# Kernel optimization log

Hardware: AMD Instinct MI355X
Metric: run time of the kernel (lower is better)

The kernel has to match this reference:

```python
import math
import jax, jax.numpy as jnp
import numpy as np

TOP_K = 2
N_EXP = 8
TRAIN_CAPACITY = 1.25
MIN_CAPACITY = 4


def _capacity(num_tokens):
    cap = math.floor(TOP_K * TRAIN_CAPACITY * num_tokens / N_EXP)
    cap += cap % 2
    return max(cap, MIN_CAPACITY)


def _router(x, w_g):
    B, T, D = x.shape
    N = B * T
    C = _capacity(N)  # static: depends only on shapes

    logits = jnp.einsum('btd,ed->bte', x, w_g)            # [B,T,E]
    _, top_idx = jax.lax.top_k(logits, TOP_K)             # [B,T,K]
    probs = jax.nn.softmax(logits, axis=-1).reshape(N, N_EXP)  # [N,E]
    idx = top_idx.reshape(N, TOP_K)                       # [N,K]

    # one-hot expert mask, laid out [K, N, E] as in the torch code
    exp_mask = jax.nn.one_hot(idx, N_EXP, dtype=jnp.int32)      # [N,K,E]
    exp_mask = jnp.transpose(exp_mask, (1, 0, 2))               # [K,N,E]

    # position of each routed token within its expert's queue
    rank = jnp.cumsum(exp_mask.reshape(TOP_K * N, N_EXP), axis=0)
    rank = rank.reshape(TOP_K, N, N_EXP) - 1                    # [K,N,E]

    exp_mask = exp_mask * (rank < C).astype(jnp.int32)          # drop over-capacity
    used_capacity = jnp.sum(exp_mask, axis=(0, 1))              # [E]
    rank_sel = jnp.sum(exp_mask * rank, axis=-1)                # [K,N] int

    idx_kn = jnp.transpose(idx)                                 # [K,N]
    keep = jnp.take_along_axis(exp_mask, idx_kn[:, :, None], axis=2)[..., 0]  # [K,N]
    p_sel = jnp.transpose(jnp.take_along_axis(probs, idx, axis=1))            # [K,N]
    w = keep.astype(probs.dtype) * p_sel                        # [K,N]

    # cb_weight[n, e, c] = sum_k exp_weights[k,n,e] * one_hot(rank_sel)[k,n,c]
    # implemented as a direct scatter-add instead of materializing the
    # O(K*N*E*C) outer product (dropped tokens contribute weight 0).
    tok = jnp.arange(N)
    cb_weight = jnp.zeros((N, N_EXP, C), probs.dtype)
    cb_weight = cb_weight.at[tok[None, :], idx_kn, rank_sel].add(w)
    sec_mask = cb_weight != 0
    return used_capacity, cb_weight, sec_mask


def setup_inputs() -> dict:
    key = jax.random.key(0)
    kx, kw = jax.random.split(key)
    x = jax.random.normal(kx, (2, 2048, 1024), dtype=jnp.float32)
    w_g = jax.random.normal(kw, (8, 1024), dtype=jnp.float32) * 0.02
    return {"x": x, "w_g": w_g}


def reference(x, w_g):
    return _router(x, w_g)
```

## Files before the change

### kernel.cpp

```cpp
#include <hip/hip_runtime.h>

#define N_TOK 4096
#define DIM   1024
#define NE    8
#define CAP   1280
#define EC    (NE * CAP)
#define NEC   ((size_t)N_TOK * EC)

__global__ __launch_bounds__(256) void k_logits(const float* __restrict__ x,
                                                const float* __restrict__ wg,
                                                int* __restrict__ top_idx,
                                                float* __restrict__ top_p) {
    __shared__ float swg[NE * DIM];
    const float4* wg4 = (const float4*)wg;
    float4* swg4 = (float4*)swg;
#pragma unroll
    for (int i = 0; i < 8; ++i) {
        int t = i * 256 + threadIdx.x;
        swg4[t] = wg4[t];
    }
    __syncthreads();

    const int wave = threadIdx.x >> 6;
    const int lane = threadIdx.x & 63;
    const int token = blockIdx.x * 4 + wave;

    const float4* x4 = (const float4*)(x + (size_t)token * DIM);
    float acc[NE];
#pragma unroll
    for (int e = 0; e < NE; ++e) acc[e] = 0.f;

#pragma unroll
    for (int c = 0; c < 4; ++c) {
        float4 xv = x4[c * 64 + lane];
#pragma unroll
        for (int e = 0; e < NE; ++e) {
            float4 wv = swg4[e * 256 + c * 64 + lane];
            acc[e] += xv.x * wv.x + xv.y * wv.y + xv.z * wv.z + xv.w * wv.w;
        }
    }
#pragma unroll
    for (int e = 0; e < NE; ++e) {
        float v = acc[e];
#pragma unroll
        for (int off = 32; off > 0; off >>= 1)
            v += __shfl_xor(v, off, 64);
        acc[e] = v;
    }

    if (lane == 0) {
        float m = acc[0];
#pragma unroll
        for (int e = 1; e < NE; ++e) m = fmaxf(m, acc[e]);
        float pe[NE];
        float s = 0.f;
#pragma unroll
        for (int e = 0; e < NE; ++e) { pe[e] = expf(acc[e] - m); s += pe[e]; }
        float inv = 1.f / s;

        int i1 = 0; float v1 = acc[0];
#pragma unroll
        for (int e = 1; e < NE; ++e) if (acc[e] > v1) { v1 = acc[e]; i1 = e; }
        int i2 = (i1 == 0) ? 1 : 0; float v2 = acc[i2];
#pragma unroll
        for (int e = 0; e < NE; ++e)
            if (e != i1 && acc[e] > v2) { v2 = acc[e]; i2 = e; }

        top_idx[token]         = i1;
        top_idx[N_TOK + token] = i2;
        top_p[token]           = pe[i1] * inv;
        top_p[N_TOK + token]   = pe[i2] * inv;
    }
}

__global__ __launch_bounds__(256) void k_rank(const int* __restrict__ top_idx,
                                              int* __restrict__ dest,
                                              float* __restrict__ used) {
    __shared__ int se[2 * N_TOK];
    __shared__ int wsum[4][NE];
    const int t = threadIdx.x;
    const int lane = t & 63;
    const int wave = t >> 6;

    const int4* ti4 = (const int4*)top_idx;
    int4* se4 = (int4*)se;
#pragma unroll
    for (int i = 0; i < 8; ++i)
        se4[i * 256 + t] = ti4[i * 256 + t];
    __syncthreads();

    int cnt[NE];
#pragma unroll
    for (int e = 0; e < NE; ++e) cnt[e] = 0;
    const int base = t * 32;
#pragma unroll
    for (int jj = 0; jj < 32; ++jj) {
        int v = se[base + jj];
#pragma unroll
        for (int e = 0; e < NE; ++e) cnt[e] += (v == e) ? 1 : 0;
    }

    int incl[NE];
#pragma unroll
    for (int e = 0; e < NE; ++e) {
        int s = cnt[e];
#pragma unroll
        for (int off = 1; off < 64; off <<= 1) {
            int u = __shfl_up(s, off, 64);
            if (lane >= off) s += u;
        }
        incl[e] = s;
        if (lane == 63) wsum[wave][e] = s;
    }
    __syncthreads();

    int excl[NE];
#pragma unroll
    for (int e = 0; e < NE; ++e) {
        int off = 0;
#pragma unroll
        for (int w = 0; w < 4; ++w)
            off += (w < wave) ? wsum[w][e] : 0;
        excl[e] = off + incl[e] - cnt[e];
    }
    if (t < NE) {
        int total = wsum[0][t] + wsum[1][t] + wsum[2][t] + wsum[3][t];
        used[t] = (float)min(total, CAP);
    }

    int run[NE];
#pragma unroll
    for (int e = 0; e < NE; ++e) run[e] = excl[e];
#pragma unroll
    for (int jj = 0; jj < 32; ++jj) {
        int j = base + jj;
        int v = se[j];
        int r = run[0];
#pragma unroll
        for (int e = 1; e < NE; ++e) r = (v == e) ? run[e] : r;
#pragma unroll
        for (int e = 0; e < NE; ++e) run[e] += (v == e) ? 1 : 0;
        dest[j] = (r < CAP) ? (v * CAP + r) : -1;
    }
}

__global__ __launch_bounds__(256) void k_scatter(const int* __restrict__ dest,
                                                 const float* __restrict__ top_p,
                                                 const float* __restrict__ used,
                                                 float* __restrict__ out) {
    const int j = blockIdx.x * 256 + threadIdx.x;
    if (blockIdx.x == 0 && threadIdx.x < NE) out[threadIdx.x] = used[threadIdx.x];

    const int d = dest[j];
    if (d >= 0) {
        const int n = j & (N_TOK - 1);
        const float w = top_p[j];
        out[8 + (size_t)n * EC + d]       = w;
        out[8 + NEC + (size_t)n * EC + d] = (w != 0.f) ? 1.f : 0.f;
    }
}

extern "C" void kernel_launch(void* const* d_in, const int* in_sizes, int n_in,
                              void* d_out, int out_size, void* d_ws, size_t ws_size,
                              hipStream_t stream) {
    const float* x  = (const float*)d_in[0];
    const float* wg = (const float*)d_in[1];
    float* out = (float*)d_out;
    char* ws = (char*)d_ws;

    int*   top_idx = (int*)(ws);
    float* top_p   = (float*)(ws + 32768);
    int*   dest    = (int*)(ws + 65536);
    float* used    = (float*)(ws + 98304);

    hipMemsetAsync(out, 0, (size_t)(8 + 2 * NEC) * sizeof(float), stream);

    k_logits<<<N_TOK / 4, 256, 0, stream>>>(x, wg, top_idx, top_p);
    k_rank<<<1, 256, 0, stream>>>(top_idx, dest, used);
    k_scatter<<<2 * N_TOK / 256, 256, 0, stream>>>(dest, top_p, used, out);
}
```

Before: 356.4 us.

## Fuse output zero-fill into logits kernel and merge rank with scatter

Replaces the hipMemsetAsync of the large output with a zero-fill done by 2048 blocks of the logits kernel, where the first 1024 blocks also compute the router logits. The rank and scatter kernels are merged into one single-block kernel that keeps destinations in shared memory. The goal is to cut launch count and overlap the bandwidth-bound zero fill with the logits compute. In exchange, the fill pattern is hand-sized and the scatter now runs in a single block, which serialises about 8K stores.

```diff
diff --git a/kernel.cpp b/kernel.cpp
--- a/kernel.cpp
+++ b/kernel.cpp
@@ -7,76 +7,99 @@
 #define EC    (NE * CAP)
 #define NEC   ((size_t)N_TOK * EC)
 
-__global__ __launch_bounds__(256) void k_logits(const float* __restrict__ x,
-                                                const float* __restrict__ wg,
-                                                int* __restrict__ top_idx,
-                                                float* __restrict__ top_p) {
+#define NB_FILL   2048
+#define F4_TOTAL  ((2 * NEC + 8) / 4)
+#define F4_BLOCK  (40 * 256)
+#define F4_MAIN   ((size_t)NB_FILL * F4_BLOCK)
+
+typedef float nt_float4 __attribute__((ext_vector_type(4)));
+
+__global__ __launch_bounds__(256) void k_fill_logits(const float* __restrict__ x,
+                                                     const float* __restrict__ wg,
+                                                     int* __restrict__ top_idx,
+                                                     float* __restrict__ top_p,
+                                                     float* __restrict__ out) {
     __shared__ float swg[NE * DIM];
-    const float4* wg4 = (const float4*)wg;
-    float4* swg4 = (float4*)swg;
+    const int bid = blockIdx.x;
+    const int tid = threadIdx.x;
+
+    if (bid < N_TOK / 4) {
+        const float4* wg4 = (const float4*)wg;
+        float4* swg4 = (float4*)swg;
 #pragma unroll
-    for (int i = 0; i < 8; ++i) {
-        int t = i * 256 + threadIdx.x;
-        swg4[t] = wg4[t];
-    }
-    __syncthreads();
+        for (int i = 0; i < 8; ++i) {
+            int t = i * 256 + tid;
+            swg4[t] = wg4[t];
+        }
+        __syncthreads();
 
-    const int wave = threadIdx.x >> 6;
-    const int lane = threadIdx.x & 63;
-    const int token = blockIdx.x * 4 + wave;
+        const int wave = tid >> 6;
+        const int lane = tid & 63;
+        const int token = bid * 4 + wave;
 
-    const float4* x4 = (const float4*)(x + (size_t)token * DIM);
-    float acc[NE];
+        const float4* x4 = (const float4*)(x + (size_t)token * DIM);
+        float acc[NE];
 #pragma unroll
-    for (int e = 0; e < NE; ++e) acc[e] = 0.f;
+        for (int e = 0; e < NE; ++e) acc[e] = 0.f;
 
 #pragma unroll
-    for (int c = 0; c < 4; ++c) {
-        float4 xv = x4[c * 64 + lane];
+        for (int c = 0; c < 4; ++c) {
+            float4 xv = x4[c * 64 + lane];
+#pragma unroll
+            for (int e = 0; e < NE; ++e) {
+                float4 wv = swg4[e * 256 + c * 64 + lane];
+                acc[e] += xv.x * wv.x + xv.y * wv.y + xv.z * wv.z + xv.w * wv.w;
+            }
+        }
 #pragma unroll
         for (int e = 0; e < NE; ++e) {
-            float4 wv = swg4[e * 256 + c * 64 + lane];
-            acc[e] += xv.x * wv.x + xv.y * wv.y + xv.z * wv.z + xv.w * wv.w;
+            float v = acc[e];
+#pragma unroll
+            for (int off = 32; off > 0; off >>= 1)
+                v += __shfl_xor(v, off, 64);
+            acc[e] = v;
+        }
+
+        if (lane == 0) {
+            float m = acc[0];
+#pragma unroll
+            for (int e = 1; e < NE; ++e) m = fmaxf(m, acc[e]);
+            float pe[NE];
+            float s = 0.f;
+#pragma unroll
+            for (int e = 0; e < NE; ++e) { pe[e] = expf(acc[e] - m); s += pe[e]; }
+            float inv = 1.f / s;
+
+            int i1 = 0; float v1 = acc[0];
+#pragma unroll
+            for (int e = 1; e < NE; ++e) if (acc[e] > v1) { v1 = acc[e]; i1 = e; }
+            int i2 = (i1 == 0) ? 1 : 0; float v2 = acc[i2];
+#pragma unroll
+            for (int e = 0; e < NE; ++e)
+                if (e != i1 && acc[e] > v2) { v2 = acc[e]; i2 = e; }
+
+            top_idx[token]         = i1;
+            top_idx[N_TOK + token] = i2;
+            top_p[token]           = pe[i1] * inv;
+            top_p[N_TOK + token]   = pe[i2] * inv;
         }
     }
+
+    nt_float4 z = (nt_float4)0.f;
+    nt_float4* o4 = (nt_float4*)out;
+    const size_t base = (size_t)bid * F4_BLOCK + tid;
 #pragma unroll
-    for (int e = 0; e < NE; ++e) {
-        float v = acc[e];
-#pragma unroll
-        for (int off = 32; off > 0; off >>= 1)
-            v += __shfl_xor(v, off, 64);
-        acc[e] = v;
-    }
-
-    if (lane == 0) {
-        float m = acc[0];
-#pragma unroll
-        for (int e = 1; e < NE; ++e) m = fmaxf(m, acc[e]);
-        float pe[NE];
-        float s = 0.f;
-#pragma unroll
-        for (int e = 0; e < NE; ++e) { pe[e] = expf(acc[e] - m); s += pe[e]; }
-        float inv = 1.f / s;
-
-        int i1 = 0; float v1 = acc[0];
-#pragma unroll
-        for (int e = 1; e < NE; ++e) if (acc[e] > v1) { v1 = acc[e]; i1 = e; }
-        int i2 = (i1 == 0) ? 1 : 0; float v2 = acc[i2];
-#pragma unroll
-        for (int e = 0; e < NE; ++e)
-            if (e != i1 && acc[e] > v2) { v2 = acc[e]; i2 = e; }
-
-        top_idx[token]         = i1;
-        top_idx[N_TOK + token] = i2;
-        top_p[token]           = pe[i1] * inv;
-        top_p[N_TOK + token]   = pe[i2] * inv;
-    }
+    for (int i = 0; i < 40; ++i)
+        o4[base + i * 256] = z;
+    if (bid == 0 && tid < (int)(F4_TOTAL - F4_MAIN))
+        o4[F4_MAIN + tid] = z;
 }
 
-__global__ __launch_bounds__(256) void k_rank(const int* __restrict__ top_idx,
-                                              int* __restrict__ dest,
-                                              float* __restrict__ used) {
+__global__ __launch_bounds__(256) void k_rank_scatter(const int* __restrict__ top_idx,
+                                                      const float* __restrict__ top_p,
+                                                      float* __restrict__ out) {
     __shared__ int se[2 * N_TOK];
+    __shared__ int sdest[2 * N_TOK];
     __shared__ int wsum[4][NE];
     const int t = threadIdx.x;
     const int lane = t & 63;
@@ -125,7 +148,7 @@
     }
     if (t < NE) {
         int total = wsum[0][t] + wsum[1][t] + wsum[2][t] + wsum[3][t];
-        used[t] = (float)min(total, CAP);
+        out[t] = (float)min(total, CAP);
     }
 
     int run[NE];
@@ -140,23 +163,20 @@
         for (int e = 1; e < NE; ++e) r = (v == e) ? run[e] : r;
 #pragma unroll
         for (int e = 0; e < NE; ++e) run[e] += (v == e) ? 1 : 0;
-        dest[j] = (r < CAP) ? (v * CAP + r) : -1;
+        sdest[j] = (r < CAP) ? (v * CAP + r) : -1;
     }
-}
+    __syncthreads();
 
-__global__ __launch_bounds__(256) void k_scatter(const int* __restrict__ dest,
-                                                 const float* __restrict__ top_p,
-                                                 const float* __restrict__ used,
-                                                 float* __restrict__ out) {
-    const int j = blockIdx.x * 256 + threadIdx.x;
-    if (blockIdx.x == 0 && threadIdx.x < NE) out[threadIdx.x] = used[threadIdx.x];
-
-    const int d = dest[j];
-    if (d >= 0) {
-        const int n = j & (N_TOK - 1);
-        const float w = top_p[j];
-        out[8 + (size_t)n * EC + d]       = w;
-        out[8 + NEC + (size_t)n * EC + d] = (w != 0.f) ? 1.f : 0.f;
+#pragma unroll
+    for (int jj = 0; jj < 32; ++jj) {
+        int j = jj * 256 + t;
+        int d = sdest[j];
+        if (d >= 0) {
+            int n = j & (N_TOK - 1);
+            float w = top_p[j];
+            out[8 + (size_t)n * EC + d]       = w;
+            out[8 + NEC + (size_t)n * EC + d] = (w != 0.f) ? 1.f : 0.f;
+        }
     }
 }
 
@@ -170,12 +190,7 @@
 
     int*   top_idx = (int*)(ws);
     float* top_p   = (float*)(ws + 32768);
-    int*   dest    = (int*)(ws + 65536);
-    float* used    = (float*)(ws + 98304);
 
-    hipMemsetAsync(out, 0, (size_t)(8 + 2 * NEC) * sizeof(float), stream);
-
-    k_logits<<<N_TOK / 4, 256, 0, stream>>>(x, wg, top_idx, top_p);
-    k_rank<<<1, 256, 0, stream>>>(top_idx, dest, used);
-    k_scatter<<<2 * N_TOK / 256, 256, 0, stream>>>(dest, top_p, used, out);
+    k_fill_logits<<<NB_FILL, 256, 0, stream>>>(x, wg, top_idx, top_p, out);
+    k_rank_scatter<<<1, 256, 0, stream>>>(top_idx, top_p, out);
 }
```

After: 373.6 us. 1.05x slower.
